# Kernel tuning notes

Hardware: AMD Instinct MI355X
Metric: run time of the kernel (lower is better)

Reference implementation:

```python
import jax, jax.numpy as jnp
import numpy as np
from jax import lax

PATCH = 8

def setup_inputs() -> dict:
    key = jax.random.key(0)
    ks = jax.random.split(key, 5)
    x = jax.random.normal(ks[0], (4, 64, 256, 256), dtype=jnp.float32)
    w_in = jax.random.normal(ks[1], (512, 64), dtype=jnp.float32) * 0.02
    b_in = jnp.zeros((512,), dtype=jnp.float32)
    w_dw = jax.random.normal(ks[2], (512, 1, 3, 3), dtype=jnp.float32) * 0.02
    b_dw = jnp.zeros((512,), dtype=jnp.float32)
    w_out = jax.random.normal(ks[3], (64, 256), dtype=jnp.float32) * 0.02
    b_out = jnp.zeros((64,), dtype=jnp.float32)
    fft_filter = jnp.ones((64, 1, 1, PATCH, PATCH // 2 + 1), dtype=jnp.float32)
    return {"x": x, "w_in": w_in, "b_in": b_in, "w_dw": w_dw, "b_dw": b_dw,
            "w_out": w_out, "b_out": b_out, "fft_filter": fft_filter}

def reference(x, w_in, b_in, w_dw, b_dw, w_out, b_out, fft_filter):
    # project_in: 1x1 conv == channel GEMM. x: [B, C, H, W] -> [B, 2h, H, W]
    h = jnp.einsum('oc,bchw->bohw', w_in, x) + b_in[None, :, None, None]
    # depthwise 3x3 conv, padding=1
    h = lax.conv_general_dilated(
        h, w_dw, window_strides=(1, 1), padding='SAME',
        dimension_numbers=('NCHW', 'OIHW', 'NCHW'),
        feature_group_count=w_dw.shape[0]) + b_dw[None, :, None, None]
    x1, x2 = jnp.split(h, 2, axis=1)
    h = jax.nn.gelu(x1, approximate=False) * x2  # exact GELU like F.gelu
    # project_out: 1x1 conv
    y = jnp.einsum('oc,bchw->bohw', w_out, h) + b_out[None, :, None, None]
    # patch-wise spectral filtering
    B, C, H, W = y.shape
    p = PATCH
    yp = y.reshape(B, C, H // p, p, W // p, p).transpose(0, 1, 2, 4, 3, 5)  # b c h w p1 p2
    yf = jnp.fft.rfft2(yp)              # b c h w p1 (p2//2+1)
    yf = yf * fft_filter                # filter broadcasts over (c,1,1,p1,p2r)
    yp = jnp.fft.irfft2(yf, s=(p, p))
    y = yp.transpose(0, 1, 2, 4, 3, 5).reshape(B, C, H, W)
    return y
```

## Files before the change

kernel.cpp:

```cpp
#include <hip/hip_runtime.h>
#include <math.h>

typedef __attribute__((ext_vector_type(8))) short short8;
typedef __attribute__((ext_vector_type(4))) float f32x4;
typedef __attribute__((ext_vector_type(2))) float f32x2;

#define TX 16
#define TY 8
#define IH 256
#define IW 256

#define WSA_OFF 16384
#define WSC_OFF 81920

#define H_ROWB 176
#define H_PLANE 1760
#define G_OFF 28160
#define SMEM_BYTES 44544

#define SP2(c) ((f32x2){(c), (c)})

__device__ __forceinline__ unsigned short f2bf(float f) {
  unsigned int u = __builtin_bit_cast(unsigned int, f);
  u = (u + 0x7FFFu + ((u >> 16) & 1u)) >> 16;
  return (unsigned short)u;
}

__global__ void edffn_prep(const float* __restrict__ fftf,
                           const float* __restrict__ w_in,
                           const float* __restrict__ w_out,
                           float* __restrict__ ws) {
  int blk = blockIdx.x, t = threadIdx.x;
  if (blk < 64) {
    int a = t >> 3, bb = t & 7;
    const float c0 = 0.70710678118654752f;
    const float ctab[8] = {1.f, c0, 0.f, -c0, -1.f, -c0, 0.f, c0};
    const float* F = fftf + blk * 40;
    float acc = 0.f;
    for (int k1 = 0; k1 < 8; ++k1)
      for (int k2 = 0; k2 < 8; ++k2) {
        float f = (k2 <= 4) ? F[k1 * 5 + k2] : F[((8 - k1) & 7) * 5 + (8 - k2)];
        acc += f * ctab[(k1 * a + k2 * bb) & 7];
      }
    ws[blk * 64 + t] = acc * (1.f / 64.f);
  } else if (blk < 128) {
    int b2 = blk - 64;
    int q = b2 >> 2, s = (b2 >> 1) & 1, ks = b2 & 1;
    int row = (s ? 256 : 0) + q * 16 + (t & 15);
    unsigned short* dst =
        (unsigned short*)((unsigned char*)ws + WSA_OFF) + (((q * 2 + s) * 2 + ks) * 64 + t) * 8;
    for (int j = 0; j < 8; ++j) {
      int k = ks * 32 + (t >> 4) * 8 + j;
      dst[j] = f2bf(w_in[row * 64 + k]);
    }
  } else {
    int b3 = blk - 128;
    int p = b3 >> 2, mt = b3 & 3;
    int row = mt * 16 + (t & 15);
    unsigned short* dst =
        (unsigned short*)((unsigned char*)ws + WSC_OFF) + ((p * 4 + mt) * 64 + t) * 8;
    for (int j = 0; j < 8; ++j) {
      int k = p * 32 + (t >> 4) * 8 + j;
      dst[j] = f2bf(w_out[row * 256 + k]);
    }
  }
}

__global__ __launch_bounds__(256, 2) void edffn_main(
    const float* __restrict__ x, const float* __restrict__ b_in,
    const float* __restrict__ w_dw, const float* __restrict__ b_dw,
    const float* __restrict__ b_out, const float* __restrict__ ws,
    float* __restrict__ out) {
  __shared__ __align__(16) unsigned char smem[SMEM_BYTES];
  __shared__ int s_flag;
  const int t = threadIdx.x;
  const int lane = t & 63, wave = t >> 6;
  const int l15 = lane & 15, lg = lane >> 4;
  const int gx0 = blockIdx.x * TX, gy0 = blockIdx.y * TY;
  const int b = blockIdx.z;
  const unsigned short* wsA = (const unsigned short*)((const unsigned char*)ws + WSA_OFF);
  const unsigned short* wsC = (const unsigned short*)((const unsigned char*)ws + WSC_OFF);

  short8 xf[3][2];
  int haddr[3];
  unsigned vmask = 0, imask = 0;
  const float* xb = x + (size_t)b * 64 * 65536;
#pragma unroll
  for (int i = 0; i < 3; ++i) {
    int nt = wave + 4 * i;
    int n = nt * 16 + l15;
    int hy = n / 18;
    int hx = n - hy * 18;
    int gy = gy0 + hy - 1, gx = gx0 + hx - 1;
    int vnt = n < 180;
    int inb = vnt & (gy >= 0) & (gy < IH) & (gx >= 0) & (gx < IW);
    haddr[i] = hy * H_ROWB + hx * 8;
    vmask |= (unsigned)vnt << i;
    imask |= (unsigned)inb << i;
    int gyc = min(max(gy, 0), IH - 1), gxc = min(max(gx, 0), IW - 1);
    const float* xp = xb + (size_t)gyc * IW + gxc;
#pragma unroll
    for (int ks = 0; ks < 2; ++ks) {
#pragma unroll
      for (int j = 0; j < 8; ++j) {
        int k = ks * 32 + lg * 8 + j;
        unsigned short bf = f2bf(xp[(size_t)k * 65536]);
        xf[i][ks][j] = (short)(inb ? bf : (unsigned short)0);
      }
    }
  }

  f32x4 accY[8];
#pragma unroll
  for (int i = 0; i < 8; ++i) accY[i] = (f32x4){0.f, 0.f, 0.f, 0.f};

  const int cp_dw = t >> 4;
  const int oy_dw = (t & 15) >> 1;
  const int h_dw = t & 1;

  auto loadAF = [&](int qq, short8 (&af)[2][2], float (&bin)[2][4]) {
#pragma unroll
    for (int s = 0; s < 2; ++s) {
#pragma unroll
      for (int ks = 0; ks < 2; ++ks)
        af[s][ks] = *(const short8*)(wsA + (((qq * 2 + s) * 2 + ks) * 64 + lane) * 8);
#pragma unroll
      for (int r = 0; r < 4; ++r) bin[s][r] = b_in[(s ? 256 : 0) + qq * 16 + lg * 4 + r];
    }
  };
  auto loadWD = [&](int qq, f32x2 (&wd)[9], f32x2& bd) {
    const int cg1 = qq * 16 + cp_dw, cg2 = 256 + qq * 16 + cp_dw;
#pragma unroll
    for (int u = 0; u < 9; ++u) wd[u] = (f32x2){w_dw[cg1 * 9 + u], w_dw[cg2 * 9 + u]};
    bd = (f32x2){b_dw[cg1], b_dw[cg2]};
  };

  short8 afC[2][2], afN[2][2];
  float binC[2][4], binN[2][4];
  f32x2 wdC[9], wdN[9], bdC, bdN;
  short8 cfC;

  loadAF(0, afC, binC);
  loadWD(0, wdC, bdC);
  cfC = *(const short8*)(wsC + ((0 * 4 + wave) * 64 + lane) * 8);

  for (int q = 0; q < 16; ++q) {
    if (q < 15) {
      loadAF(q + 1, afN, binN);
      loadWD(q + 1, wdN, bdN);
    }

    {
#pragma unroll
      for (int i = 0; i < 3; ++i) {
        f32x4 acc0 = {0.f, 0.f, 0.f, 0.f}, acc1 = {0.f, 0.f, 0.f, 0.f};
        acc0 = __builtin_amdgcn_mfma_f32_16x16x32_bf16(afC[0][0], xf[i][0], acc0, 0, 0, 0);
        acc0 = __builtin_amdgcn_mfma_f32_16x16x32_bf16(afC[0][1], xf[i][1], acc0, 0, 0, 0);
        acc1 = __builtin_amdgcn_mfma_f32_16x16x32_bf16(afC[1][0], xf[i][0], acc1, 0, 0, 0);
        acc1 = __builtin_amdgcn_mfma_f32_16x16x32_bf16(afC[1][1], xf[i][1], acc1, 0, 0, 0);
        if ((vmask >> i) & 1u) {
          unsigned keep = (imask >> i) & 1u;
#pragma unroll
          for (int r = 0; r < 4; ++r) {
            f32x2 hv = (f32x2){acc0[r] + binC[0][r], acc1[r] + binC[1][r]};
            if (!keep) hv = (f32x2){0.f, 0.f};
            *(f32x2*)(smem + (lg * 4 + r) * H_PLANE + haddr[i]) = hv;
          }
        }
      }
    }
    __syncthreads();

    {
      const int cp = cp_dw, oy = oy_dw, h = h_dw;
      f32x2 a[8];
#pragma unroll
      for (int j = 0; j < 8; ++j) a[j] = bdC;
#pragma unroll
      for (int dy = 0; dy < 3; ++dy) {
        const unsigned char* base = smem + cp * H_PLANE + (oy + dy) * H_ROWB + h * 64;
        f32x2 e[10];
#pragma unroll
        for (int i5 = 0; i5 < 5; ++i5) {
          f32x4 v = *(const f32x4*)(base + i5 * 16);
          e[2 * i5] = (f32x2){v[0], v[1]};
          e[2 * i5 + 1] = (f32x2){v[2], v[3]};
        }
#pragma unroll
        for (int ox = 0; ox < 8; ++ox) {
#pragma unroll
          for (int dx = 0; dx < 3; ++dx)
            a[ox] = __builtin_elementwise_fma(wdC[dy * 3 + dx], e[ox + dx], a[ox]);
        }
      }
      const int c2 = (q & 1) * 16 + cp;
      const int gi = (c2 >> 3) ^ (oy & 3);
      unsigned short* Gp =
          (unsigned short*)(smem + G_OFF) + oy * 16 * 32 + gi * 8 + (c2 & 7);
#pragma unroll
      for (int j = 0; j < 4; ++j) {
        f32x2 u = (f32x2){a[2 * j][0], a[2 * j + 1][0]};
        f32x2 v = (f32x2){a[2 * j][1], a[2 * j + 1][1]};
        f32x2 z = u * 0.70710678118654752f;
        f32x2 z2 = z * z;
        f32x2 erfv;
        if (__builtin_expect(fmaxf(z2[0], z2[1]) > 0.16f, 0)) {
          erfv[0] = erff(z[0]);
          erfv[1] = erff(z[1]);
        } else {
          f32x2 p = __builtin_elementwise_fma(z2, SP2(1.f / 216.f), SP2(-1.f / 42.f));
          p = __builtin_elementwise_fma(z2, p, SP2(1.f / 10.f));
          p = __builtin_elementwise_fma(z2, p, SP2(-1.f / 3.f));
          p = __builtin_elementwise_fma(z2, p, SP2(1.f));
          erfv = 1.12837916709551257f * (z * p);
        }
        f32x2 tt = __builtin_elementwise_fma(erfv, SP2(0.5f), SP2(0.5f));
        f32x2 g = (u * tt) * v;
        Gp[(h * 8 + 2 * j) * 32] = f2bf(g[0]);
        Gp[(h * 8 + 2 * j + 1) * 32] = f2bf(g[1]);
      }
    }
    __syncthreads();

    if (q & 1) {
      const int p = q >> 1;
      const unsigned short* G = (const unsigned short*)(smem + G_OFF);
#pragma unroll
      for (int nt = 0; nt < 8; ++nt) {
        int g = lg ^ (nt & 3);
        int n = nt * 16 + l15;
        short8 bf = *(const short8*)(G + n * 32 + g * 8);
        accY[nt] = __builtin_amdgcn_mfma_f32_16x16x32_bf16(cfC, bf, accY[nt], 0, 0, 0);
      }
      if (q < 15)
        cfC = *(const short8*)(wsC + (((p + 1) * 4 + wave) * 64 + lane) * 8);
    }

    if (q < 15) {
#pragma unroll
      for (int s = 0; s < 2; ++s) {
#pragma unroll
        for (int ks = 0; ks < 2; ++ks) afC[s][ks] = afN[s][ks];
#pragma unroll
        for (int r = 0; r < 4; ++r) binC[s][r] = binN[s][r];
      }
#pragma unroll
      for (int u = 0; u < 9; ++u) wdC[u] = wdN[u];
      bdC = bdN;
    }
  }

  {
    f32x4 bo;
#pragma unroll
    for (int r = 0; r < 4; ++r) bo[r] = b_out[wave * 16 + lg * 4 + r];
#pragma unroll
    for (int nt = 0; nt < 8; ++nt)
#pragma unroll
      for (int r = 0; r < 4; ++r) accY[nt][r] += bo[r];
  }

  if (t == 0) s_flag = 1;
  __syncthreads();
  {
    int ok = 1;
    const float* kc = ws;
#pragma unroll
    for (int j = 0; j < 16; ++j) {
      int idx = t * 16 + j;
      float e = ((idx & 63) == 0) ? 1.f : 0.f;
      ok &= (fabsf(kc[idx] - e) <= 1e-5f) ? 1 : 0;
    }
    if (!ok) s_flag = 0;
  }
  __syncthreads();

  const int o = wave * 16 + lg * 4;
  if (s_flag) {
#pragma unroll
    for (int nt = 0; nt < 8; ++nt) {
      float* op = out + (((size_t)(b * 64 + o)) * IH + gy0 + nt) * IW + gx0 + l15;
#pragma unroll
      for (int r = 0; r < 4; ++r) op[(size_t)r * IH * IW] = accY[nt][r];
    }
    return;
  }

  float* YS = (float*)smem;
  for (int half = 0; half < 2; ++half) {
    __syncthreads();
    if ((wave >> 1) == half) {
      int c32 = (wave & 1) * 16 + lg * 4;
#pragma unroll
      for (int nt = 0; nt < 8; ++nt)
#pragma unroll
        for (int r = 0; r < 4; ++r) YS[(c32 + r) * 132 + nt * 16 + l15] = accY[nt][r];
    }
    __syncthreads();
    if (t < 64) {
      int o32 = t >> 1, oo = half * 32 + o32, qd = t & 1;
      const float* kp = ws + oo * 64;
      int px0 = qd * 8;
      const float* row = YS + o32 * 132;
      for (int i = 0; i < 8; ++i)
        for (int j = 0; j < 8; ++j) {
          float acc = 0.f;
          for (int a_ = 0; a_ < 8; ++a_)
            for (int b_ = 0; b_ < 8; ++b_)
              acc += kp[a_ * 8 + b_] *
                     row[((i - a_) & 7) * 16 + px0 + ((j - b_) & 7)];
          out[(((size_t)(b * 64 + oo)) * IH + gy0 + i) * IW + gx0 + px0 + j] = acc;
        }
    }
  }
}

extern "C" void kernel_launch(void* const* d_in, const int* in_sizes, int n_in,
                              void* d_out, int out_size, void* d_ws, size_t ws_size,
                              hipStream_t stream) {
  const float* x = (const float*)d_in[0];
  const float* w_in = (const float*)d_in[1];
  const float* b_in = (const float*)d_in[2];
  const float* w_dw = (const float*)d_in[3];
  const float* b_dw = (const float*)d_in[4];
  const float* w_out = (const float*)d_in[5];
  const float* b_out = (const float*)d_in[6];
  const float* fftf = (const float*)d_in[7];
  float* out = (float*)d_out;
  float* ws = (float*)d_ws;

  edffn_prep<<<160, 64, 0, stream>>>(fftf, w_in, w_out, ws);
  dim3 grid(IW / TX, IH / TY, 4);
  edffn_main<<<grid, 256, 0, stream>>>(x, b_in, w_dw, b_dw, b_out, ws, out);
}
```

Measured before the change: 173.3 us.

## Store intermediate in fp16, use packed f16 FMA for depthwise conv, prefetch GEMM

The project-in result is packed to fp16 pairs in registers and stored to LDS at half the footprint. The depthwise 3x3 conv now uses v_pk_fma_f16 on these pairs. The next q-step's MFMA GEMM is computed right after the barrier, so it overlaps the depthwise and GELU work, and afC/binC are no longer needed. The aim is less LDS traffic and footprint, fewer VALU ops and more overlap, at the cost of fp16 accuracy with round-toward-zero conversion in the conv accumulation.

```diff
diff --git a/kernel.cpp b/kernel.cpp
--- a/kernel.cpp
+++ b/kernel.cpp
@@ -13,10 +13,9 @@
 #define WSA_OFF 16384
 #define WSC_OFF 81920
 
-#define H_ROWB 176
-#define H_PLANE 1760
-#define G_OFF 28160
-#define SMEM_BYTES 44544
+#define H_STRIDE 816
+#define G_OFF 13056
+#define SMEM_BYTES 29440
 
 #define SP2(c) ((f32x2){(c), (c)})
 
@@ -94,7 +93,7 @@
     int gy = gy0 + hy - 1, gx = gx0 + hx - 1;
     int vnt = n < 180;
     int inb = vnt & (gy >= 0) & (gy < IH) & (gx >= 0) & (gx < IW);
-    haddr[i] = hy * H_ROWB + hx * 8;
+    haddr[i] = hy * 80 + hx * 4;
     vmask |= (unsigned)vnt << i;
     imask |= (unsigned)inb << i;
     int gyc = min(max(gy, 0), IH - 1), gxc = min(max(gx, 0), IW - 1);
@@ -118,79 +117,93 @@
   const int oy_dw = (t & 15) >> 1;
   const int h_dw = t & 1;
 
-  auto loadAF = [&](int qq, short8 (&af)[2][2], float (&bin)[2][4]) {
+  short8 afN[2][2];
+  float binN[2][4];
+  unsigned wdC[9], wdN[9], bdC, bdN;
+  short8 cfC;
+  unsigned ha[3][4];
+
+  auto loadAF = [&](int qq) {
 #pragma unroll
     for (int s = 0; s < 2; ++s) {
 #pragma unroll
       for (int ks = 0; ks < 2; ++ks)
-        af[s][ks] = *(const short8*)(wsA + (((qq * 2 + s) * 2 + ks) * 64 + lane) * 8);
-#pragma unroll
-      for (int r = 0; r < 4; ++r) bin[s][r] = b_in[(s ? 256 : 0) + qq * 16 + lg * 4 + r];
+        afN[s][ks] = *(const short8*)(wsA + (((qq * 2 + s) * 2 + ks) * 64 + lane) * 8);
+#pragma unroll
+      for (int r = 0; r < 4; ++r) binN[s][r] = b_in[(s ? 256 : 0) + qq * 16 + lg * 4 + r];
     }
   };
-  auto loadWD = [&](int qq, f32x2 (&wd)[9], f32x2& bd) {
+  auto loadWD = [&](int qq, unsigned (&wd)[9], unsigned& bd) {
     const int cg1 = qq * 16 + cp_dw, cg2 = 256 + qq * 16 + cp_dw;
 #pragma unroll
-    for (int u = 0; u < 9; ++u) wd[u] = (f32x2){w_dw[cg1 * 9 + u], w_dw[cg2 * 9 + u]};
-    bd = (f32x2){b_dw[cg1], b_dw[cg2]};
+    for (int u = 0; u < 9; ++u) {
+      float w1 = w_dw[cg1 * 9 + u], w2 = w_dw[cg2 * 9 + u];
+      asm("v_cvt_pkrtz_f16_f32 %0, %1, %2" : "=v"(wd[u]) : "v"(w1), "v"(w2));
+    }
+    float b1 = b_dw[cg1], b2 = b_dw[cg2];
+    asm("v_cvt_pkrtz_f16_f32 %0, %1, %2" : "=v"(bd) : "v"(b1), "v"(b2));
   };
-
-  short8 afC[2][2], afN[2][2];
-  float binC[2][4], binN[2][4];
-  f32x2 wdC[9], wdN[9], bdC, bdN;
-  short8 cfC;
-
-  loadAF(0, afC, binC);
+  auto computeA = [&]() {
+#pragma unroll
+    for (int i = 0; i < 3; ++i) {
+      f32x4 acc0 = {0.f, 0.f, 0.f, 0.f}, acc1 = {0.f, 0.f, 0.f, 0.f};
+      acc0 = __builtin_amdgcn_mfma_f32_16x16x32_bf16(afN[0][0], xf[i][0], acc0, 0, 0, 0);
+      acc0 = __builtin_amdgcn_mfma_f32_16x16x32_bf16(afN[0][1], xf[i][1], acc0, 0, 0, 0);
+      acc1 = __builtin_amdgcn_mfma_f32_16x16x32_bf16(afN[1][0], xf[i][0], acc1, 0, 0, 0);
+      acc1 = __builtin_amdgcn_mfma_f32_16x16x32_bf16(afN[1][1], xf[i][1], acc1, 0, 0, 0);
+      unsigned keep = (imask >> i) & 1u;
+#pragma unroll
+      for (int r = 0; r < 4; ++r) {
+        float v0 = acc0[r] + binN[0][r];
+        float v1 = acc1[r] + binN[1][r];
+        unsigned pk;
+        asm("v_cvt_pkrtz_f16_f32 %0, %1, %2" : "=v"(pk) : "v"(v0), "v"(v1));
+        ha[i][r] = keep ? pk : 0u;
+      }
+    }
+  };
+
+  loadAF(0);
   loadWD(0, wdC, bdC);
   cfC = *(const short8*)(wsC + ((0 * 4 + wave) * 64 + lane) * 8);
+  computeA();
 
   for (int q = 0; q < 16; ++q) {
+#pragma unroll
+    for (int i = 0; i < 3; ++i) {
+      if ((vmask >> i) & 1u) {
+#pragma unroll
+        for (int r = 0; r < 4; ++r)
+          *(unsigned*)(smem + (lg * 4 + r) * H_STRIDE + haddr[i]) = ha[i][r];
+      }
+    }
     if (q < 15) {
-      loadAF(q + 1, afN, binN);
+      loadAF(q + 1);
       loadWD(q + 1, wdN, bdN);
     }
-
-    {
-#pragma unroll
-      for (int i = 0; i < 3; ++i) {
-        f32x4 acc0 = {0.f, 0.f, 0.f, 0.f}, acc1 = {0.f, 0.f, 0.f, 0.f};
-        acc0 = __builtin_amdgcn_mfma_f32_16x16x32_bf16(afC[0][0], xf[i][0], acc0, 0, 0, 0);
-        acc0 = __builtin_amdgcn_mfma_f32_16x16x32_bf16(afC[0][1], xf[i][1], acc0, 0, 0, 0);
-        acc1 = __builtin_amdgcn_mfma_f32_16x16x32_bf16(afC[1][0], xf[i][0], acc1, 0, 0, 0);
-        acc1 = __builtin_amdgcn_mfma_f32_16x16x32_bf16(afC[1][1], xf[i][1], acc1, 0, 0, 0);
-        if ((vmask >> i) & 1u) {
-          unsigned keep = (imask >> i) & 1u;
-#pragma unroll
-          for (int r = 0; r < 4; ++r) {
-            f32x2 hv = (f32x2){acc0[r] + binC[0][r], acc1[r] + binC[1][r]};
-            if (!keep) hv = (f32x2){0.f, 0.f};
-            *(f32x2*)(smem + (lg * 4 + r) * H_PLANE + haddr[i]) = hv;
-          }
-        }
-      }
-    }
     __syncthreads();
+
+    if (q < 15) computeA();
 
     {
       const int cp = cp_dw, oy = oy_dw, h = h_dw;
-      f32x2 a[8];
+      unsigned a[8];
 #pragma unroll
       for (int j = 0; j < 8; ++j) a[j] = bdC;
 #pragma unroll
       for (int dy = 0; dy < 3; ++dy) {
-        const unsigned char* base = smem + cp * H_PLANE + (oy + dy) * H_ROWB + h * 64;
-        f32x2 e[10];
-#pragma unroll
-        for (int i5 = 0; i5 < 5; ++i5) {
-          f32x4 v = *(const f32x4*)(base + i5 * 16);
-          e[2 * i5] = (f32x2){v[0], v[1]};
-          e[2 * i5 + 1] = (f32x2){v[2], v[3]};
-        }
+        const unsigned char* base = smem + cp * H_STRIDE + (oy + dy) * 80 + h * 32;
+        uint4 r0 = *(const uint4*)base;
+        uint4 r1 = *(const uint4*)(base + 16);
+        uint2 r2 = *(const uint2*)(base + 32);
+        unsigned e[10] = {r0.x, r0.y, r0.z, r0.w, r1.x, r1.y, r1.z, r1.w, r2.x, r2.y};
 #pragma unroll
         for (int ox = 0; ox < 8; ++ox) {
 #pragma unroll
           for (int dx = 0; dx < 3; ++dx)
-            a[ox] = __builtin_elementwise_fma(wdC[dy * 3 + dx], e[ox + dx], a[ox]);
+            asm("v_pk_fma_f16 %0, %1, %2, %0"
+                : "+v"(a[ox])
+                : "v"(wdC[dy * 3 + dx]), "v"(e[ox + dx]));
         }
       }
       const int c2 = (q & 1) * 16 + cp;
@@ -199,8 +212,13 @@
           (unsigned short*)(smem + G_OFF) + oy * 16 * 32 + gi * 8 + (c2 & 7);
 #pragma unroll
       for (int j = 0; j < 4; ++j) {
-        f32x2 u = (f32x2){a[2 * j][0], a[2 * j + 1][0]};
-        f32x2 v = (f32x2){a[2 * j][1], a[2 * j + 1][1]};
+        unsigned a0 = a[2 * j], a1 = a[2 * j + 1];
+        unsigned a0h = a0 >> 16, a1h = a1 >> 16;
+        f32x2 u, v;
+        asm("v_cvt_f32_f16 %0, %1" : "=v"(u[0]) : "v"(a0));
+        asm("v_cvt_f32_f16 %0, %1" : "=v"(u[1]) : "v"(a1));
+        asm("v_cvt_f32_f16 %0, %1" : "=v"(v[0]) : "v"(a0h));
+        asm("v_cvt_f32_f16 %0, %1" : "=v"(v[1]) : "v"(a1h));
         f32x2 z = u * 0.70710678118654752f;
         f32x2 z2 = z * z;
         f32x2 erfv;
@@ -238,13 +256,6 @@
 
     if (q < 15) {
 #pragma unroll
-      for (int s = 0; s < 2; ++s) {
-#pragma unroll
-        for (int ks = 0; ks < 2; ++ks) afC[s][ks] = afN[s][ks];
-#pragma unroll
-        for (int r = 0; r < 4; ++r) binC[s][r] = binN[s][r];
-      }
-#pragma unroll
       for (int u = 0; u < 9; ++u) wdC[u] = wdN[u];
       bdC = bdN;
     }
```

Result: slower. 183.7 us (+5.9%).
